# Kernel optimization log

Measured on AMD Instinct MI355X. Metric: run time of the kernel, lower is better.

Reference implementation:

```python
import jax, jax.numpy as jnp
import numpy as np

B, N, K, H, E_DIM = 2, 1024, 48, 128, 128
NUM_IN = E_DIM + H          # 256
CAT = H + NUM_IN            # 384, input dim of W1/W11
FF = 4 * H                  # 512, PositionWiseFeedForward hidden
SCALE = 48.0                # EncoderLayer scale arg
LN_EPS = 1e-5


def _lin(x, w, b):
    # w: [in, out]
    return x @ w + b


def _ln(x, g, b):
    m = x.mean(-1, keepdims=True)
    v = ((x - m) ** 2).mean(-1, keepdims=True)
    return (x - m) * jax.lax.rsqrt(v + LN_EPS) * g + b


def _gelu(x):
    return jax.nn.gelu(x, approximate=False)  # torch.nn.GELU default = exact erf


def setup_inputs() -> dict:
    key = jax.random.key(0)
    ks = iter(jax.random.split(key, 40))

    def nrm(shape, scale=1.0):
        return (jax.random.normal(next(ks), shape, dtype=jnp.float32) * scale)

    def lin_p(din, dout):
        s = 1.0 / np.sqrt(din)
        return nrm((din, dout), s), nrm((dout,), s)

    inp = {
        'h_V': nrm((B, N, H)),
        'h_E': nrm((B, N, K, E_DIM)),
        'E_idx': jax.random.randint(next(ks), (B, N, K), 0, N, dtype=jnp.int64),
        'mask_V': jnp.ones((B, N), dtype=jnp.float32),
        'mask_attend': jnp.ones((B, N, K), dtype=jnp.float32),
    }
    for name, (din, dout) in [('W1', (CAT, H)), ('W2', (H, H)), ('W3', (H, H)),
                              ('W11', (CAT, H)), ('W12', (H, H)), ('W13', (H, H)),
                              ('Win', (H, FF)), ('Wout', (FF, H))]:
        w, b = lin_p(din, dout)
        inp[name + '_w'] = w
        inp[name + '_b'] = b
    for ln in ['ln1', 'ln2', 'ln3']:
        inp[ln + '_g'] = jnp.ones((H,), dtype=jnp.float32)
        inp[ln + '_b'] = jnp.zeros((H,), dtype=jnp.float32)
    return inp


def reference(h_V, h_E, E_idx, mask_V, mask_attend,
              W1_w, W1_b, W2_w, W2_b, W3_w, W3_b,
              W11_w, W11_b, W12_w, W12_b, W13_w, W13_b,
              Win_w, Win_b, Wout_w, Wout_b,
              ln1_g, ln1_b, ln2_g, ln2_b, ln3_g, ln3_b):
    b_idx = jnp.arange(h_V.shape[0])[:, None, None]  # [B,1,1]

    def gather_nodes(nodes):
        # nodes [B,N,H] -> neighbor features [B,N,K,H]
        return nodes[b_idx, E_idx]

    def build_hEV(hv):
        hv_nb = gather_nodes(hv)                                  # [B,N,K,H]
        hv_ex = jnp.broadcast_to(hv[:, :, None, :], hv_nb.shape)  # [B,N,K,H]
        return jnp.concatenate([hv_ex, h_E, hv_nb], axis=-1)       # [B,N,K,384]

    # --- node message: W3(gelu(W2(gelu(W1(h_EV))))) ---
    m = _lin(_gelu(_lin(_gelu(_lin(build_hEV(h_V), W1_w, W1_b)), W2_w, W2_b)), W3_w, W3_b)
    m = mask_attend[..., None] * m
    dh = m.sum(axis=-2) / SCALE                     # [B,N,H]
    h_Vn = _ln(h_V + dh, ln1_g, ln1_b)              # dropout = identity (eval)

    # --- position-wise FFN ---
    dh = _lin(_gelu(_lin(h_Vn, Win_w, Win_b)), Wout_w, Wout_b)
    h_Vn = _ln(h_Vn + dh, ln2_g, ln2_b)
    h_Vn = mask_V[..., None] * h_Vn

    # --- edge message: W13(gelu(W12(gelu(W11(h_EV))))) with updated h_V ---
    me = _lin(_gelu(_lin(_gelu(_lin(build_hEV(h_Vn), W11_w, W11_b)), W12_w, W12_b)), W13_w, W13_b)
    h_En = _ln(h_E + me, ln3_g, ln3_b)

    return h_Vn, h_En
```

## Files before the change

kernel.cpp:

```cpp
#include <hip/hip_runtime.h>
#include <cstdint>
#include <cstddef>

typedef unsigned short u16;
typedef unsigned int   u32;
typedef __bf16  bf16x8 __attribute__((ext_vector_type(8)));
typedef float   f32x4  __attribute__((ext_vector_type(4)));

#define B_    2
#define N_    1024
#define K_    48
#define H_    128
#define CAT_  384
#define FF_   512
#define YPAD  136
#define HIDP  520
#define MPAD  132
#define MSP   68
#define XAP   264
#define EPS_  1e-5f
#define INV_SCALE (1.0f/48.0f)

__device__ __forceinline__ float bf2f(u16 u){ u32 x=((u32)u)<<16; float f; __builtin_memcpy(&f,&x,4); return f; }
__device__ __forceinline__ u16 f2bf(float f){ u32 x; __builtin_memcpy(&x,&f,4); x=(x+0x7FFFu+((x>>16)&1u))>>16; return (u16)x; }
__device__ __forceinline__ u32 pk2(float lo, float hi){ return (u32)f2bf(lo) | ((u32)f2bf(hi)<<16); }

__device__ __forceinline__ float gelu_ex(float x){
    const float s = x * 0.7071067811865476f;
    const float a = fabsf(s);
    const float t = __builtin_amdgcn_rcpf(__builtin_fmaf(0.3275911f, a, 1.0f));
    float p = __builtin_fmaf(1.061405429f, t, -1.453152027f);
    p = __builtin_fmaf(p, t,  1.421413741f);
    p = __builtin_fmaf(p, t, -0.284496736f);
    p = __builtin_fmaf(p, t,  0.254829592f);
    p *= t;
    const float e = __expf(-s*s);
    const float erfa = __builtin_fmaf(-p, e, 1.0f);
    const float erf  = __builtin_copysignf(erfa, s);
    return 0.5f*x*(1.0f+erf);
}
__device__ __forceinline__ f32x4 fzero(){ f32x4 v; v[0]=0.f; v[1]=0.f; v[2]=0.f; v[3]=0.f; return v; }

__device__ __forceinline__ float ldf(const void* p, size_t i, int bf){
    return bf ? bf2f(((const u16*)p)[i]) : ((const float*)p)[i];
}
__device__ __forceinline__ void cp8(u16* dst, const void* src, size_t eoff, int bf){
    if (bf) { *(uint4*)dst = *(const uint4*)((const u16*)src + eoff); }
    else {
        const float4* s = (const float4*)((const float*)src + eoff);
        float4 a = s[0], b = s[1];
        uint4 o; o.x = pk2(a.x,a.y); o.y = pk2(a.z,a.w); o.z = pk2(b.x,b.y); o.w = pk2(b.z,b.w);
        *(uint4*)dst = o;
    }
}

__device__ __forceinline__ int probe_f_par(const void* p, int n_elems, int tid,
                                           volatile int* s_spec, volatile int* s_nb)
{
    if (tid == 0) {
        const u32 w0 = ((const u32*)p)[0];
        *s_spec = (w0 == 0x3F803F80u) ? 1 : ((w0 == 0x3F800000u) ? 0 : -1);
        *s_nb = 0;
    }
    __syncthreads();
    int sp = *s_spec;
    if (sp < 0) {
        const int m = n_elems < 128 ? n_elems : 128;
        if (tid < m) {
            float v = fabsf(bf2f(((const u16*)p)[tid]));
            if (v > 1e6f) *s_nb = 1;
        }
        __syncthreads();
        sp = (*s_nb) ? 0 : 1;
    }
    __syncthreads();
    return sp;
}
__device__ __forceinline__ int probe_i_par(const int* p, int tid, volatile int* s_nb)
{
    if (tid == 0) *s_nb = 0;
    __syncthreads();
    if (tid < 128) { if (((const u32*)p)[2*tid+1] != 0u) *s_nb = 1; }
    __syncthreads();
    const int r = (*s_nb) ? 0 : 1;
    __syncthreads();
    return r;
}
struct Ptrs27 { const void* p[27]; int n[27]; };

__global__ void __launch_bounds__(256)
mega_prep(Ptrs27 P, u16* __restrict__ ws, int* __restrict__ flags, float* __restrict__ gv1f)
{
    u16* w1t   = ws;
    u16* w2t   = w1t   + 128*384;
    u16* w3t   = w2t   + 128*128;
    u16* w11t  = w3t   + 128*128;
    u16* w12t  = w11t  + 128*384;
    u16* w13t  = w12t  + 128*128;
    u16* wintt = w13t  + 128*128;
    u16* woutt = wintt + 512*128;
    int* idxn  = (int*)(woutt + 128*512);

    __shared__ int s_spec, s_nb;
    __shared__ __align__(16) u16 smem[144*136];
    const int blk = blockIdx.x;
    const int tid = threadIdx.x;

    if (blk >= 483) {
        const int r0g = (blk - 483) * 16;
        const int fHV = probe_f_par(P.p[0], P.n[0], tid, &s_spec, &s_nb);
        const int fW1 = probe_f_par(P.p[5], P.n[5], tid, &s_spec, &s_nb);
        const int fb1 = probe_f_par(P.p[6], P.n[6], tid, &s_spec, &s_nb);
        u16* Wt = smem;
        u16* Ah = smem + 128*136;
        {
            const int row = tid >> 4, c8 = (tid & 15) << 3;
            cp8(&Ah[row*136 + c8], P.p[0], (size_t)(r0g+row)*H_ + c8, fHV);
        }
        {
            const void* w1src = P.p[5];
            for (int e = tid; e < 128*128; e += 256) {
                const int k = e >> 7, n = e & 127;
                Wt[n*136 + k] = fW1 ? ((const u16*)w1src)[k*128 + n]
                                    : f2bf(((const float*)w1src)[(size_t)k*128 + n]);
            }
        }
        __syncthreads();
        const int lane = tid & 63, w = tid >> 6;
        const int l15 = lane & 15, q = lane >> 4;
        const int n0 = w*32;
        f32x4 a0v, a1v;
        { float b0v = ldf(P.p[6], n0+l15, fb1), b1v = ldf(P.p[6], n0+16+l15, fb1);
          for (int r=0;r<4;r++){ a0v[r]=b0v; a1v[r]=b1v; } }
#pragma unroll 1
        for (int k0 = 0; k0 < H_; k0 += 32) {
            const int ko = k0 + q*8;
            bf16x8 a  = *(const bf16x8*)&Ah[l15*136 + ko];
            bf16x8 b0 = *(const bf16x8*)&Wt[(n0 + l15)*136 + ko];
            bf16x8 b1 = *(const bf16x8*)&Wt[(n0 + 16 + l15)*136 + ko];
            a0v = __builtin_amdgcn_mfma_f32_16x16x32_bf16(a,b0,a0v,0,0,0);
            a1v = __builtin_amdgcn_mfma_f32_16x16x32_bf16(a,b1,a1v,0,0,0);
        }
        for (int r=0;r<4;r++) {
            gv1f[(size_t)(r0g + q*4 + r)*H_ + n0 + l15]      = a0v[r];
            gv1f[(size_t)(r0g + q*4 + r)*H_ + n0 + 16 + l15] = a1v[r];
        }
        return;
    }
    if (blk >= 456) {
        const int t = blk - 456;
        const int r = (t == 2) ? probe_i_par((const int*)P.p[t], tid, &s_nb)
                               : probe_f_par(P.p[t], P.n[t], tid, &s_spec, &s_nb);
        if (tid == 0) flags[t] = r;
        return;
    }
    if (blk >= 72) {
        const int* s = (const int*)P.p[2];
        const int w64 = probe_i_par(s, tid, &s_nb);
        const int i = (blk - 72)*256 + tid;
        if (i < B_*N_*K_) idxn[i] = w64 ? s[2*i] : s[i];
        return;
    }
    u16 (*tile)[65] = (u16(*)[65])smem;
    const void* src; u16* dst; int ri, co, rel;
    if      (blk < 12) { src=P.p[5];  dst=w1t;   ri=384; co=128; rel=blk;     }
    else if (blk < 16) { src=P.p[7];  dst=w2t;   ri=128; co=128; rel=blk-12;  }
    else if (blk < 20) { src=P.p[9];  dst=w3t;   ri=128; co=128; rel=blk-16;  }
    else if (blk < 32) { src=P.p[11]; dst=w11t;  ri=384; co=128; rel=blk-20;  }
    else if (blk < 36) { src=P.p[13]; dst=w12t;  ri=128; co=128; rel=blk-32;  }
    else if (blk < 40) { src=P.p[15]; dst=w13t;  ri=128; co=128; rel=blk-36;  }
    else if (blk < 56) { src=P.p[17]; dst=wintt; ri=128; co=512; rel=blk-40;  }
    else               { src=P.p[19]; dst=woutt; ri=512; co=128; rel=blk-56;  }
    const int bf = probe_f_par(src, 128, tid, &s_spec, &s_nb);
    const int tc = co >> 6;
    const int r0 = (rel / tc) * 64, o0 = (rel % tc) * 64;
    const int lr = tid >> 6, lc = tid & 63;
#pragma unroll
    for (int pph = 0; pph < 16; pph++) {
        const int row = pph*4 + lr;
        tile[row][lc] = bf ? ((const u16*)src)[(size_t)(r0+row)*co + o0 + lc]
                           : f2bf(((const float*)src)[(size_t)(r0+row)*co + o0 + lc]);
    }
    __syncthreads();
#pragma unroll
    for (int pph = 0; pph < 16; pph++) {
        const int o = pph*4 + lr;
        dst[(size_t)(o0+o)*ri + r0 + lc] = tile[lc][o];
    }
}

template<int KD, int AP, int LD, int KOFF>
__device__ __forceinline__ void mfma3x1(const u16* As, const u16* __restrict__ wt, int tid, int ct, f32x4 acc[3])
{
    const int lane = tid & 63;
    const int l15  = lane & 15, q = lane >> 4;
    const int n0   = (tid >> 6) * 32 + ct*16;
#pragma unroll 2
    for (int k0 = 0; k0 < KD; k0 += 32) {
        const int ko = k0 + q*8;
        bf16x8 b0 = *(const bf16x8*)&wt[(size_t)(n0 + l15)*LD + KOFF + ko];
        bf16x8 a0 = *(const bf16x8*)&As[(l15     )*AP + ko];
        bf16x8 a1 = *(const bf16x8*)&As[(l15 + 16)*AP + ko];
        bf16x8 a2 = *(const bf16x8*)&As[(l15 + 32)*AP + ko];
        acc[0] = __builtin_amdgcn_mfma_f32_16x16x32_bf16(a0,b0,acc[0],0,0,0);
        acc[1] = __builtin_amdgcn_mfma_f32_16x16x32_bf16(a1,b0,acc[1],0,0,0);
        acc[2] = __builtin_amdgcn_mfma_f32_16x16x32_bf16(a2,b0,acc[2],0,0,0);
    }
}
template<bool BIAS>
__device__ __forceinline__ void epi_gelu1(const f32x4 acc[3], const void* __restrict__ bias, int bf,
                                          u16* Outs, int tid, int ct)
{
    const int lane = tid & 63, l15 = lane & 15, q = lane >> 4;
    const int col = (tid>>6)*32 + ct*16 + l15;
    float bv = 0.f;
    if constexpr (BIAS) bv = ldf(bias, col, bf);
    for (int mt = 0; mt < 3; mt++)
        for (int r = 0; r < 4; r++)
            Outs[(mt*16 + q*4 + r)*YPAD + col] = f2bf(gelu_ex(acc[mt][r] + bv));
}

__global__ void __launch_bounds__(256, 4)
node_mfma(const void* __restrict__ hV, const void* __restrict__ hE, const int* __restrict__ idxn,
          const void* __restrict__ maskAtt,
          const u16* __restrict__ w1t,
          const u16* __restrict__ w2t, const void* __restrict__ b2,
          const u16* __restrict__ w3t, const void* __restrict__ b3,
          const void* __restrict__ g1, const void* __restrict__ be1,
          const float* __restrict__ gv1f,
          const int* __restrict__ flags,
          float* __restrict__ hvn1f)
{
    __shared__ __align__(16) u16 Xs[K_*XAP];
    __shared__ __align__(16) u16 Y1s[K_*YPAD];
    __shared__ float dhs[H_];
    __shared__ float matt[K_];
    __shared__ int   idxs[K_];
    __shared__ float stats[3];

    const int bn  = blockIdx.x;
    const int b   = bn >> 10;
    const int tid = threadIdx.x;
    const int lane = tid & 63, w = tid >> 6;

    const int fHV = flags[0], fHE = flags[1], fMA = flags[4];
    const int fb2 = flags[8], fb3 = flags[10];
    const int fg1 = flags[21], fbe1 = flags[22];

    if (tid < K_) { idxs[tid] = idxn[bn*K_ + tid]; matt[tid] = ldf(maskAtt, (size_t)bn*K_ + tid, fMA); }
    __syncthreads();
    if (tid == 0) { float s=0.f; for (int k=0;k<K_;k++) s += matt[k]; stats[2] = s; }

    for (int u = tid; u < 768; u += 256) {
        const int row = u >> 4, c8 = (u & 15) << 3;
        cp8(&Xs[row*XAP + c8],      hE, ((size_t)bn*K_ + row)*H_ + c8, fHE);
        cp8(&Xs[row*XAP + H_ + c8], hV, ((size_t)b*N_ + idxs[row])*H_ + c8, fHV);
    }
    __syncthreads();

    const int l15 = lane & 15, q = lane >> 4, n0 = w*32;

#pragma unroll 1
    for (int ct = 0; ct < 2; ct++) {
        f32x4 acc[3];
        const float g = gv1f[(size_t)bn*H_ + n0 + ct*16 + l15];
        for (int mt=0; mt<3; mt++) for (int r=0; r<4; r++) acc[mt][r] = g;
        mfma3x1<256, XAP, CAT_, H_>(Xs, w1t, tid, ct, acc);
        epi_gelu1<false>(acc, nullptr, 0, Y1s, tid, ct);
    }
    __syncthreads();

    u16* Y2s = Xs;
#pragma unroll 1
    for (int ct = 0; ct < 2; ct++) {
        f32x4 acc[3] = {fzero(), fzero(), fzero()};
        mfma3x1<H_, YPAD, H_, 0>(Y1s, w2t, tid, ct, acc);
        epi_gelu1<true>(acc, b2, fb2, Y2s, tid, ct);
    }
    __syncthreads();

#pragma unroll 1
    for (int ct = 0; ct < 2; ct++) {
        f32x4 acc[3] = {fzero(), fzero(), fzero()};
        mfma3x1<H_, YPAD, H_, 0>(Y2s, w3t, tid, ct, acc);
        float s0 = 0.f;
        for (int mt=0; mt<3; mt++)
            for (int r=0; r<4; r++)
                s0 += acc[mt][r]*matt[mt*16 + q*4 + r];
        s0 += __shfl_xor(s0,16); s0 += __shfl_xor(s0,32);
        if (q == 0) {
            const int col = n0 + ct*16 + l15;
            dhs[col] = (s0 + ldf(b3, col, fb3)*stats[2]) * INV_SCALE;
        }
    }
    __syncthreads();

    if (w == 0) {
        float a = ldf(hV, (size_t)bn*H_ + lane,      fHV) + dhs[lane];
        float c = ldf(hV, (size_t)bn*H_ + lane + 64, fHV) + dhs[lane+64];
        float s = a + c, ss = a*a + c*c;
        for (int off=32; off>0; off>>=1) { s += __shfl_xor(s,off); ss += __shfl_xor(ss,off); }
        if (lane == 0) { float m = s*(1.f/H_); stats[0]=m; stats[1]=rsqrtf(ss*(1.f/H_)-m*m+EPS_); }
    }
    __syncthreads();
    if (tid < H_) {
        float h = ldf(hV, (size_t)bn*H_ + tid, fHV) + dhs[tid];
        hvn1f[(size_t)bn*H_ + tid] = (h - stats[0])*stats[1]*ldf(g1,tid,fg1) + ldf(be1,tid,fbe1);
    }
}

__global__ void __launch_bounds__(256, 2)
ffn_fused(const float* __restrict__ hvn1f, const void* __restrict__ maskV,
          const u16* __restrict__ wintt, const void* __restrict__ bin,
          const u16* __restrict__ woutt, const void* __restrict__ bout,
          const u16* __restrict__ w11t, const void* __restrict__ b11,
          const void* __restrict__ g2, const void* __restrict__ be2,
          const int* __restrict__ flags,
          float* __restrict__ outV, u16* __restrict__ wsVn, float* __restrict__ gv11f)
{
    __shared__ __align__(16) float hvf[16*H_];
    __shared__ __align__(16) u16   Xh[16*YPAD];
    __shared__ __align__(16) u16   hid[16*HIDP];
    __shared__ __align__(16) float h2f[16*MPAD];
    __shared__ __align__(16) u16   h2b[16*YPAD];

    const int r0  = blockIdx.x*16;
    const int tid = threadIdx.x, lane = tid & 63, w = tid >> 6;
    const int l15 = lane & 15, q = lane >> 4;
    const int fMV = flags[3], fbin = flags[18], fbout = flags[20];
    const int fb11 = flags[12], fg2 = flags[23], fbe2 = flags[24];

    {
        const int row = tid >> 4, c8 = (tid & 15) << 3;
        const float4* s = (const float4*)&hvn1f[(size_t)(r0+row)*H_ + c8];
        float4 a = s[0], b = s[1];
        *(float4*)&hvf[row*H_ + c8]     = a;
        *(float4*)&hvf[row*H_ + c8 + 4] = b;
        uint4 o; o.x = pk2(a.x,a.y); o.y = pk2(a.z,a.w); o.z = pk2(b.x,b.y); o.w = pk2(b.z,b.w);
        *(uint4*)&Xh[row*YPAD + c8] = o;
    }
    __syncthreads();

    {
        f32x4 acc[8];
#pragma unroll
        for (int ct = 0; ct < 8; ct++) {
            const float bv = ldf(bin, w*128 + ct*16 + l15, fbin);
            for (int r=0;r<4;r++) acc[ct][r] = bv;
        }
#pragma unroll 1
        for (int k0 = 0; k0 < H_; k0 += 32) {
            const int ko = k0 + q*8;
            bf16x8 a = *(const bf16x8*)&Xh[l15*YPAD + ko];
#pragma unroll
            for (int ct = 0; ct < 8; ct++) {
                bf16x8 b = *(const bf16x8*)&wintt[(size_t)(w*128 + ct*16 + l15)*H_ + ko];
                acc[ct] = __builtin_amdgcn_mfma_f32_16x16x32_bf16(a,b,acc[ct],0,0,0);
            }
        }
#pragma unroll
        for (int ct = 0; ct < 8; ct++) {
            const int col = w*128 + ct*16 + l15;
            for (int r=0;r<4;r++)
                hid[(q*4 + r)*HIDP + col] = f2bf(gelu_ex(acc[ct][r]));
        }
    }
    __syncthreads();

    {
        const int n0 = w*32;
        f32x4 c0 = fzero(), c1 = fzero();
#pragma unroll 1
        for (int k0 = 0; k0 < FF_; k0 += 32) {
            const int ko = k0 + q*8;
            bf16x8 a  = *(const bf16x8*)&hid[l15*HIDP + ko];
            bf16x8 b0 = *(const bf16x8*)&woutt[(size_t)(n0 + l15)*FF_ + ko];
            bf16x8 b1 = *(const bf16x8*)&woutt[(size_t)(n0 + 16 + l15)*FF_ + ko];
            c0 = __builtin_amdgcn_mfma_f32_16x16x32_bf16(a,b0,c0,0,0,0);
            c1 = __builtin_amdgcn_mfma_f32_16x16x32_bf16(a,b1,c1,0,0,0);
        }
        const float bo0 = ldf(bout, n0+l15, fbout), bo1 = ldf(bout, n0+16+l15, fbout);
        for (int r=0;r<4;r++) {
            const int row = q*4 + r;
            h2f[row*MPAD + n0+l15]    = c0[r] + bo0 + hvf[row*H_ + n0+l15];
            h2f[row*MPAD + n0+16+l15] = c1[r] + bo1 + hvf[row*H_ + n0+16+l15];
        }
    }
    __syncthreads();

    for (int row = w; row < 16; row += 4) {
        float v0 = h2f[row*MPAD + lane], v1 = h2f[row*MPAD + lane + 64];
        float s = v0+v1, ss = v0*v0+v1*v1;
        for (int off=32; off>0; off>>=1) { s += __shfl_xor(s,off); ss += __shfl_xor(ss,off); }
        const float m = s*(1.f/H_);
        const float rstd = rsqrtf(ss*(1.f/H_) - m*m + EPS_);
        const float mk = ldf(maskV, r0+row, fMV);
        const float o0 = ((v0-m)*rstd*ldf(g2,lane,fg2)    + ldf(be2,lane,fbe2))    * mk;
        const float o1 = ((v1-m)*rstd*ldf(g2,lane+64,fg2) + ldf(be2,lane+64,fbe2)) * mk;
        outV[(size_t)(r0+row)*H_ + lane]      = o0;
        outV[(size_t)(r0+row)*H_ + lane + 64] = o1;
        const u16 u0 = f2bf(o0), u1 = f2bf(o1);
        wsVn[(size_t)(r0+row)*H_ + lane]      = u0;
        wsVn[(size_t)(r0+row)*H_ + lane + 64] = u1;
        h2b[row*YPAD + lane]      = u0;
        h2b[row*YPAD + lane + 64] = u1;
    }
    __syncthreads();

    {
        const int n0 = w*32;
        f32x4 d0, d1;
        { float b0v = ldf(b11, n0+l15, fb11), b1v = ldf(b11, n0+16+l15, fb11);
          for (int r=0;r<4;r++){ d0[r]=b0v; d1[r]=b1v; } }
#pragma unroll 1
        for (int k0 = 0; k0 < H_; k0 += 32) {
            const int ko = k0 + q*8;
            bf16x8 a  = *(const bf16x8*)&h2b[l15*YPAD + ko];
            bf16x8 b0 = *(const bf16x8*)&w11t[(size_t)(n0 + l15)*CAT_ + ko];
            bf16x8 b1 = *(const bf16x8*)&w11t[(size_t)(n0 + 16 + l15)*CAT_ + ko];
            d0 = __builtin_amdgcn_mfma_f32_16x16x32_bf16(a,b0,d0,0,0,0);
            d1 = __builtin_amdgcn_mfma_f32_16x16x32_bf16(a,b1,d1,0,0,0);
        }
        for (int r=0;r<4;r++) {
            gv11f[(size_t)(r0 + q*4 + r)*H_ + n0 + l15]      = d0[r];
            gv11f[(size_t)(r0 + q*4 + r)*H_ + n0 + 16 + l15] = d1[r];
        }
    }
}

__global__ void __launch_bounds__(256, 4)
edge_mfma(const u16* __restrict__ wsVn, const void* __restrict__ hE, const int* __restrict__ idxn,
          const u16* __restrict__ w11t,
          const u16* __restrict__ w12t, const void* __restrict__ b12,
          const u16* __restrict__ w13t, const void* __restrict__ b13,
          const void* __restrict__ g3, const void* __restrict__ be3,
          const float* __restrict__ gv11f,
          const int* __restrict__ flags,
          float* __restrict__ outE)
{
    __shared__ __align__(16) u16 hEs[K_*YPAD];
    __shared__ __align__(16) u16 hvnbs[K_*YPAD];
    __shared__ __align__(16) u16 Y1s[K_*YPAD];
    __shared__ int idxs[K_];

    const int bn  = blockIdx.x;
    const int b   = bn >> 10;
    const int tid = threadIdx.x;
    const int lane = tid & 63, w = tid >> 6;

    const int fHE = flags[1];
    const int fb12 = flags[14], fb13 = flags[16];
    const int fg3 = flags[25], fbe3 = flags[26];

    if (tid < K_) idxs[tid] = idxn[bn*K_ + tid];
    __syncthreads();

    const u16* hVb = wsVn + (size_t)b*N_*H_;
    for (int u = tid; u < 768; u += 256) {
        const int row = u >> 4, c8 = (u & 15) << 3;
        cp8(&hEs[row*YPAD + c8], hE, ((size_t)bn*K_ + row)*H_ + c8, fHE);
        *(uint4*)&hvnbs[row*YPAD + c8] = *(const uint4*)&hVb[(size_t)idxs[row]*H_ + c8];
    }
    __syncthreads();

    const int l15 = lane & 15, q = lane >> 4, n0 = w*32;

#pragma unroll 1
    for (int ct = 0; ct < 2; ct++) {
        f32x4 acc[3];
        const float g = gv11f[(size_t)bn*H_ + n0 + ct*16 + l15];
        for (int mt=0; mt<3; mt++) for (int r=0; r<4; r++) acc[mt][r] = g;
        mfma3x1<H_, YPAD, CAT_, H_>(hEs,   w11t, tid, ct, acc);
        mfma3x1<H_, YPAD, CAT_, 2*H_>(hvnbs, w11t, tid, ct, acc);
        epi_gelu1<false>(acc, nullptr, 0, Y1s, tid, ct);
    }
    __syncthreads();

    u16* Y2s = hvnbs;
#pragma unroll 1
    for (int ct = 0; ct < 2; ct++) {
        f32x4 acc[3] = {fzero(), fzero(), fzero()};
        mfma3x1<H_, YPAD, H_, 0>(Y1s, w12t, tid, ct, acc);
        epi_gelu1<true>(acc, b12, fb12, Y2s, tid, ct);
    }
    __syncthreads();

    float* Ms0 = (float*)Y1s;
    {
        f32x4 accA[3] = {fzero(), fzero(), fzero()};
        mfma3x1<H_, YPAD, H_, 0>(Y2s, w13t, tid, 0, accA);
        const float bvA = ldf(b13, n0 + l15, fb13);
        const int ci = w*16 + l15;
        for (int mt=0; mt<3; mt++)
            for (int r=0; r<4; r++)
                Ms0[(mt*16 + q*4 + r)*MSP + ci] = accA[mt][r] + bvA;
    }
    {
        f32x4 accB[3] = {fzero(), fzero(), fzero()};
        mfma3x1<H_, YPAD, H_, 0>(Y2s, w13t, tid, 1, accB);
        __syncthreads();
        float* Ms1 = (float*)hvnbs;
        const float bvB = ldf(b13, n0 + 16 + l15, fb13);
        const int ci = w*16 + l15;
        for (int mt=0; mt<3; mt++)
            for (int r=0; r<4; r++)
                Ms1[(mt*16 + q*4 + r)*MSP + ci] = accB[mt][r] + bvB;
    }
    __syncthreads();

    {
        const float* Ms0c = (const float*)Y1s;
        const float* Ms1c = (const float*)hvnbs;
        const int g0  = lane >> 4;
        const int ci0 = (g0 >> 1)*16 + (lane & 15);
        const int ci1 = ci0 + 32;
        const float* Mt = (g0 & 1) ? Ms1c : Ms0c;
        const float gg0 = ldf(g3, lane, fg3),   gg1 = ldf(g3, lane+64, fg3);
        const float bb0 = ldf(be3, lane, fbe3), bb1 = ldf(be3, lane+64, fbe3);
        for (int row = w; row < K_; row += 4) {
            const size_t e0 = ((size_t)bn*K_ + row)*H_;
            float v0 = bf2f(hEs[row*YPAD + lane])      + Mt[row*MSP + ci0];
            float v1 = bf2f(hEs[row*YPAD + lane + 64]) + Mt[row*MSP + ci1];
            float s = v0+v1, ss = v0*v0+v1*v1;
            for (int off=32; off>0; off>>=1) { s += __shfl_xor(s,off); ss += __shfl_xor(ss,off); }
            const float m = s*(1.f/H_);
            const float rstd = rsqrtf(ss*(1.f/H_) - m*m + EPS_);
            outE[e0 + lane]      = (v0-m)*rstd*gg0 + bb0;
            outE[e0 + lane + 64] = (v1-m)*rstd*gg1 + bb1;
        }
    }
}

extern "C" void kernel_launch(void* const* d_in, const int* in_sizes, int n_in,
                              void* d_out, int out_size, void* d_ws, size_t ws_size,
                              hipStream_t stream)
{
    const void* hV      = d_in[0];
    const void* hE      = d_in[1];
    const void* maskV   = d_in[3];
    const void* maskAtt = d_in[4];
    const void* W2b  = d_in[8];
    const void* W3b  = d_in[10];
    const void* W11b = d_in[12];
    const void* W12b = d_in[14];
    const void* W13b = d_in[16];
    const void* Winb = d_in[18];
    const void* Woutb= d_in[20];
    const void* ln1g = d_in[21]; const void* ln1b = d_in[22];
    const void* ln2g = d_in[23]; const void* ln2b = d_in[24];
    const void* ln3g = d_in[25]; const void* ln3b = d_in[26];

    u16* ws    = (u16*)d_ws;
    u16* w1t   = ws;
    u16* w2t   = w1t   + 128*384;
    u16* w3t   = w2t   + 128*128;
    u16* w11t  = w3t   + 128*128;
    u16* w12t  = w11t  + 128*384;
    u16* w13t  = w12t  + 128*128;
    u16* wintt = w13t  + 128*128;
    u16* woutt = wintt + 512*128;
    int* idxn  = (int*)(woutt + 128*512);
    u16* wsVn  = (u16*)(idxn + B_*N_*K_);
    float* gv1f  = (float*)(wsVn + B_*N_*H_);
    float* hvn1f = gv1f  + (size_t)B_*N_*H_;
    float* gv11f = hvn1f + (size_t)B_*N_*H_;
    int* flags = (int*)(gv11f + (size_t)B_*N_*H_);

    Ptrs27 P;
    for (int i = 0; i < 27; i++) { P.p[i] = d_in[i]; P.n[i] = in_sizes[i]; }

    hipLaunchKernelGGL(mega_prep, dim3(611), dim3(256), 0, stream, P, ws, flags, gv1f);

    float* outV = (float*)d_out;
    float* outE = outV + (size_t)B_*N_*H_;

    hipLaunchKernelGGL(node_mfma, dim3(B_*N_), dim3(256), 0, stream,
                       hV, hE, idxn, maskAtt,
                       w1t, w2t, W2b, w3t, W3b,
                       ln1g, ln1b, gv1f, flags, hvn1f);
    hipLaunchKernelGGL(ffn_fused, dim3(B_*N_/16), dim3(256), 0, stream,
                       hvn1f, maskV, wintt, Winb, woutt, Woutb,
                       w11t, W11b, ln2g, ln2b, flags, outV, wsVn, gv11f);
    hipLaunchKernelGGL(edge_mfma, dim3(B_*N_), dim3(256), 0, stream,
                       wsVn, hE, idxn,
                       w11t, w12t, W12b, w13t, W13b,
                       ln3g, ln3b, gv11f, flags, outE);
}
```

Measured before the change: 277.6 us.

## Use 8 waves per block in node and edge kernels, one column tile each

The node and edge kernels now launch 512 threads per block instead of 256. Each wave owns a single 16-column output tile instead of looping over two, and the W13 epilogue splits odd and even waves across the two scratch buffers with a barrier in between. The aim is more wave-level parallelism and latency hiding per neighbour set. The cost is more redundant B-operand loads per block and a launch bound of 8 blocks per CU at 512 threads, which forces a low per-thread register budget. The barrier placed inside divergent branches also relies on every wave reaching some barrier.

New measurement: 270.8 us. 2.5% less time.

```diff
diff --git a/kernel.cpp b/kernel.cpp
--- a/kernel.cpp
+++ b/kernel.cpp
@@ -113,18 +113,14 @@
         const int fb1 = probe_f_par(P.p[6], P.n[6], tid, &s_spec, &s_nb);
         u16* Wt = smem;
         u16* Ah = smem + 128*136;
-        {
-            const int row = tid >> 4, c8 = (tid & 15) << 3;
-            cp8(&Ah[row*136 + c8], P.p[0], (size_t)(r0g+row)*H_ + c8, fHV);
-        }
-        {
-            const void* w1src = P.p[5];
+        {   const int row = tid >> 4, c8 = (tid & 15) << 3;
+            cp8(&Ah[row*136 + c8], P.p[0], (size_t)(r0g+row)*H_ + c8, fHV); }
+        {   const void* w1src = P.p[5];
             for (int e = tid; e < 128*128; e += 256) {
                 const int k = e >> 7, n = e & 127;
                 Wt[n*136 + k] = fW1 ? ((const u16*)w1src)[k*128 + n]
                                     : f2bf(((const float*)w1src)[(size_t)k*128 + n]);
-            }
-        }
+            } }
         __syncthreads();
         const int lane = tid & 63, w = tid >> 6;
         const int l15 = lane & 15, q = lane >> 4;
@@ -190,11 +186,9 @@
 }
 
 template<int KD, int AP, int LD, int KOFF>
-__device__ __forceinline__ void mfma3x1(const u16* As, const u16* __restrict__ wt, int tid, int ct, f32x4 acc[3])
-{
-    const int lane = tid & 63;
+__device__ __forceinline__ void mfma3w(const u16* As, const u16* __restrict__ wt, int lane, int n0, f32x4 acc[3])
+{
     const int l15  = lane & 15, q = lane >> 4;
-    const int n0   = (tid >> 6) * 32 + ct*16;
 #pragma unroll 2
     for (int k0 = 0; k0 < KD; k0 += 32) {
         const int ko = k0 + q*8;
@@ -209,10 +203,10 @@
 }
 template<bool BIAS>
 __device__ __forceinline__ void epi_gelu1(const f32x4 acc[3], const void* __restrict__ bias, int bf,
-                                          u16* Outs, int tid, int ct)
-{
-    const int lane = tid & 63, l15 = lane & 15, q = lane >> 4;
-    const int col = (tid>>6)*32 + ct*16 + l15;
+                                          u16* Outs, int lane, int n0)
+{
+    const int l15 = lane & 15, q = lane >> 4;
+    const int col = n0 + l15;
     float bv = 0.f;
     if constexpr (BIAS) bv = ldf(bias, col, bf);
     for (int mt = 0; mt < 3; mt++)
@@ -220,7 +214,7 @@
             Outs[(mt*16 + q*4 + r)*YPAD + col] = f2bf(gelu_ex(acc[mt][r] + bv));
 }
 
-__global__ void __launch_bounds__(256, 4)
+__global__ void __launch_bounds__(512, 8)
 node_mfma(const void* __restrict__ hV, const void* __restrict__ hE, const int* __restrict__ idxn,
           const void* __restrict__ maskAtt,
           const u16* __restrict__ w1t,
@@ -251,45 +245,43 @@
     __syncthreads();
     if (tid == 0) { float s=0.f; for (int k=0;k<K_;k++) s += matt[k]; stats[2] = s; }
 
-    for (int u = tid; u < 768; u += 256) {
+    for (int u = tid; u < 768; u += 512) {
         const int row = u >> 4, c8 = (u & 15) << 3;
         cp8(&Xs[row*XAP + c8],      hE, ((size_t)bn*K_ + row)*H_ + c8, fHE);
         cp8(&Xs[row*XAP + H_ + c8], hV, ((size_t)b*N_ + idxs[row])*H_ + c8, fHV);
     }
     __syncthreads();
 
-    const int l15 = lane & 15, q = lane >> 4, n0 = w*32;
-
-#pragma unroll 1
-    for (int ct = 0; ct < 2; ct++) {
+    const int l15 = lane & 15, q = lane >> 4;
+    const int n0 = w*16;
+
+    {
         f32x4 acc[3];
-        const float g = gv1f[(size_t)bn*H_ + n0 + ct*16 + l15];
+        const float g = gv1f[(size_t)bn*H_ + n0 + l15];
         for (int mt=0; mt<3; mt++) for (int r=0; r<4; r++) acc[mt][r] = g;
-        mfma3x1<256, XAP, CAT_, H_>(Xs, w1t, tid, ct, acc);
-        epi_gelu1<false>(acc, nullptr, 0, Y1s, tid, ct);
+        mfma3w<256, XAP, CAT_, H_>(Xs, w1t, lane, n0, acc);
+        epi_gelu1<false>(acc, nullptr, 0, Y1s, lane, n0);
     }
     __syncthreads();
 
     u16* Y2s = Xs;
-#pragma unroll 1
-    for (int ct = 0; ct < 2; ct++) {
+    {
         f32x4 acc[3] = {fzero(), fzero(), fzero()};
-        mfma3x1<H_, YPAD, H_, 0>(Y1s, w2t, tid, ct, acc);
-        epi_gelu1<true>(acc, b2, fb2, Y2s, tid, ct);
-    }
-    __syncthreads();
-
-#pragma unroll 1
-    for (int ct = 0; ct < 2; ct++) {
+        mfma3w<H_, YPAD, H_, 0>(Y1s, w2t, lane, n0, acc);
+        epi_gelu1<true>(acc, b2, fb2, Y2s, lane, n0);
+    }
+    __syncthreads();
+
+    {
         f32x4 acc[3] = {fzero(), fzero(), fzero()};
-        mfma3x1<H_, YPAD, H_, 0>(Y2s, w3t, tid, ct, acc);
+        mfma3w<H_, YPAD, H_, 0>(Y2s, w3t, lane, n0, acc);
         float s0 = 0.f;
         for (int mt=0; mt<3; mt++)
             for (int r=0; r<4; r++)
                 s0 += acc[mt][r]*matt[mt*16 + q*4 + r];
         s0 += __shfl_xor(s0,16); s0 += __shfl_xor(s0,32);
         if (q == 0) {
-            const int col = n0 + ct*16 + l15;
+            const int col = n0 + l15;
             dhs[col] = (s0 + ldf(b3, col, fb3)*stats[2]) * INV_SCALE;
         }
     }
@@ -428,7 +420,7 @@
     }
 }
 
-__global__ void __launch_bounds__(256, 4)
+__global__ void __launch_bounds__(512, 8)
 edge_mfma(const u16* __restrict__ wsVn, const void* __restrict__ hE, const int* __restrict__ idxn,
           const u16* __restrict__ w11t,
           const u16* __restrict__ w12t, const void* __restrict__ b12,
@@ -456,55 +448,52 @@
     __syncthreads();
 
     const u16* hVb = wsVn + (size_t)b*N_*H_;
-    for (int u = tid; u < 768; u += 256) {
+    for (int u = tid; u < 768; u += 512) {
         const int row = u >> 4, c8 = (u & 15) << 3;
         cp8(&hEs[row*YPAD + c8], hE, ((size_t)bn*K_ + row)*H_ + c8, fHE);
         *(uint4*)&hvnbs[row*YPAD + c8] = *(const uint4*)&hVb[(size_t)idxs[row]*H_ + c8];
     }
     __syncthreads();
 
-    const int l15 = lane & 15, q = lane >> 4, n0 = w*32;
-
-#pragma unroll 1
-    for (int ct = 0; ct < 2; ct++) {
+    const int l15 = lane & 15, q = lane >> 4;
+    const int n0 = w*16;
+
+    {
         f32x4 acc[3];
-        const float g = gv11f[(size_t)bn*H_ + n0 + ct*16 + l15];
+        const float g = gv11f[(size_t)bn*H_ + n0 + l15];
         for (int mt=0; mt<3; mt++) for (int r=0; r<4; r++) acc[mt][r] = g;
-        mfma3x1<H_, YPAD, CAT_, H_>(hEs,   w11t, tid, ct, acc);
-        mfma3x1<H_, YPAD, CAT_, 2*H_>(hvnbs, w11t, tid, ct, acc);
-        epi_gelu1<false>(acc, nullptr, 0, Y1s, tid, ct);
+        mfma3w<H_, YPAD, CAT_, H_>(hEs,   w11t, lane, n0, acc);
+        mfma3w<H_, YPAD, CAT_, 2*H_>(hvnbs, w11t, lane, n0, acc);
+        epi_gelu1<false>(acc, nullptr, 0, Y1s, lane, n0);
     }
     __syncthreads();
 
     u16* Y2s = hvnbs;
-#pragma unroll 1
-    for (int ct = 0; ct < 2; ct++) {
+    {
         f32x4 acc[3] = {fzero(), fzero(), fzero()};
-        mfma3x1<H_, YPAD, H_, 0>(Y1s, w12t, tid, ct, acc);
-        epi_gelu1<true>(acc, b12, fb12, Y2s, tid, ct);
-    }
-    __syncthreads();
-
-    float* Ms0 = (float*)Y1s;
-    {
-        f32x4 accA[3] = {fzero(), fzero(), fzero()};
-        mfma3x1<H_, YPAD, H_, 0>(Y2s, w13t, tid, 0, accA);
-        const float bvA = ldf(b13, n0 + l15, fb13);
-        const int ci = w*16 + l15;
-        for (int mt=0; mt<3; mt++)
-            for (int r=0; r<4; r++)
-                Ms0[(mt*16 + q*4 + r)*MSP + ci] = accA[mt][r] + bvA;
-    }
-    {
-        f32x4 accB[3] = {fzero(), fzero(), fzero()};
-        mfma3x1<H_, YPAD, H_, 0>(Y2s, w13t, tid, 1, accB);
-        __syncthreads();
-        float* Ms1 = (float*)hvnbs;
-        const float bvB = ldf(b13, n0 + 16 + l15, fb13);
-        const int ci = w*16 + l15;
-        for (int mt=0; mt<3; mt++)
-            for (int r=0; r<4; r++)
-                Ms1[(mt*16 + q*4 + r)*MSP + ci] = accB[mt][r] + bvB;
+        mfma3w<H_, YPAD, H_, 0>(Y1s, w12t, lane, n0, acc);
+        epi_gelu1<true>(acc, b12, fb12, Y2s, lane, n0);
+    }
+    __syncthreads();
+
+    {
+        f32x4 acc[3] = {fzero(), fzero(), fzero()};
+        mfma3w<H_, YPAD, H_, 0>(Y2s, w13t, lane, n0, acc);
+        const float bv = ldf(b13, n0 + l15, fb13);
+        const int ci = (w >> 1)*16 + l15;
+        if ((w & 1) == 0) {
+            float* Ms0 = (float*)Y1s;
+            for (int mt=0; mt<3; mt++)
+                for (int r=0; r<4; r++)
+                    Ms0[(mt*16 + q*4 + r)*MSP + ci] = acc[mt][r] + bv;
+            __syncthreads();
+        } else {
+            __syncthreads();
+            float* Ms1 = (float*)hvnbs;
+            for (int mt=0; mt<3; mt++)
+                for (int r=0; r<4; r++)
+                    Ms1[(mt*16 + q*4 + r)*MSP + ci] = acc[mt][r] + bv;
+        }
     }
     __syncthreads();
 
@@ -517,7 +506,7 @@
         const float* Mt = (g0 & 1) ? Ms1c : Ms0c;
         const float gg0 = ldf(g3, lane, fg3),   gg1 = ldf(g3, lane+64, fg3);
         const float bb0 = ldf(be3, lane, fbe3), bb1 = ldf(be3, lane+64, fbe3);
-        for (int row = w; row < K_; row += 4) {
+        for (int row = w; row < K_; row += 8) {
             const size_t e0 = ((size_t)bn*K_ + row)*H_;
             float v0 = bf2f(hEs[row*YPAD + lane])      + Mt[row*MSP + ci0];
             float v1 = bf2f(hEs[row*YPAD + lane + 64]) + Mt[row*MSP + ci1];
@@ -574,14 +563,14 @@
     float* outV = (float*)d_out;
     float* outE = outV + (size_t)B_*N_*H_;
 
-    hipLaunchKernelGGL(node_mfma, dim3(B_*N_), dim3(256), 0, stream,
+    hipLaunchKernelGGL(node_mfma, dim3(B_*N_), dim3(512), 0, stream,
                        hV, hE, idxn, maskAtt,
                        w1t, w2t, W2b, w3t, W3b,
                        ln1g, ln1b, gv1f, flags, hvn1f);
     hipLaunchKernelGGL(ffn_fused, dim3(B_*N_/16), dim3(256), 0, stream,
                        hvn1f, maskV, wintt, Winb, woutt, Woutb,
                        w11t, W11b, ln2g, ln2b, flags, outV, wsVn, gv11f);
-    hipLaunchKernelGGL(edge_mfma, dim3(B_*N_), dim3(256), 0, stream,
+    hipLaunchKernelGGL(edge_mfma, dim3(B_*N_), dim3(512), 0, stream,
                        wsVn, hE, idxn,
                        w11t, w12t, W12b, w13t, W13b,
                        ln3g, ln3b, gv11f, flags, outE);
```
